# Performance work log

Measured on AMD Instinct MI355X. Metric: run time of the kernel, lower is better.

## Reference

```python
import jax, jax.numpy as jnp
import numpy as np
from jax import lax

B, C, L = 2048, 9605, 8
WL_PER_LABEL = 50
ALPHA = 0.5        # training_config['alpha4']
ALPHA1 = 0.1       # margin
ALPHA2 = 2.0       # training_config['alpha2']
ALPHA3 = 10.0      # training_config['alpha3']
ALPHA_OTHER = 0.5
NEG = jnp.float32(-1e30)


def setup_inputs() -> dict:
    key = jax.random.key(0)
    k1, k2, k3, k4 = jax.random.split(key, 4)
    x = jax.random.normal(k1, (B, C), dtype=jnp.float32) * 2.0
    y = (jax.random.uniform(k2, (B, C)) < 0.005).astype(jnp.float32)
    y_neg = (jax.random.uniform(k3, (B, C)) < 0.005).astype(jnp.float32)
    # whitelist masks: L app-labels, each whitelisting ~WL_PER_LABEL raw classes
    idx = jax.random.randint(k4, (L, WL_PER_LABEL), 0, C)
    wl_masks = jnp.zeros((L, C), dtype=bool).at[jnp.arange(L)[:, None], idx].set(True)
    return {"x": x, "y": y, "y_neg": y_neg, "wl_masks": wl_masks}


def reference(x, y, y_neg, wl_masks):
    # y_neg is consumed by the original forward (find_gt_whitelist) but never
    # affects the returned loss, faithfully ignored here.
    xs_pos = jax.nn.sigmoid(x)                                  # [B, C]
    # top_k_thres = max(11th-largest sigmoid, alpha_other)
    thres = jnp.maximum(lax.top_k(xs_pos, 11)[0][:, 10], ALPHA_OTHER)  # [B]
    # per-label whitelist max: m[b,l] = max_{c in wl_l} xs_pos[b,c]
    m = jnp.max(jnp.where(wl_masks[None, :, :], xs_pos[:, None, :], NEG), axis=-1)  # [B, L]
    # label l is a ground-truth whitelist label iff y has any positive in wl_l
    has_pos = jnp.einsum('bc,lc->bl', y, wl_masks.astype(y.dtype)) > 0   # [B, L]
    correct_max = jnp.max(jnp.where(has_pos, m, NEG), axis=-1)           # [B]
    incorrect_max = jnp.max(jnp.where(~has_pos, m, NEG), axis=-1)        # [B]
    any_correct = jnp.any(has_pos, axis=-1)
    any_incorrect = jnp.any(~has_pos, axis=-1)
    # union whitelist max (the "other" branch uses xs_pos over all wl indices)
    union_max = jnp.max(jnp.where(jnp.any(wl_masks, axis=0)[None, :], xs_pos, NEG), axis=-1)
    x1 = jnp.where(any_correct, correct_max, thres)
    x2 = jnp.where(any_correct,
                   jnp.where(any_incorrect, jnp.maximum(incorrect_max, thres), thres),
                   union_max)
    coef = jnp.where(any_correct, 1.0, 1.0 - ALPHA)
    d = x2 - x1 + ALPHA1
    rank = jnp.where(d > 0, ALPHA2, 1.0) * jax.nn.sigmoid(ALPHA3 * d)
    return jnp.mean(coef * rank)
```

## Files before the change

kernel.cpp:

```cpp
#include <hip/hip_runtime.h>

#define CC 9605
#define BB 2048
#define LL 8
#define CAND_MAX 384
#define NEGF (-1e30f)

#define WS_PARTIALS_OFF 16384

__device__ __forceinline__ unsigned enc_f(float f) {
  unsigned u = __float_as_uint(f);
  return (u & 0x80000000u) ? ~u : (u | 0x80000000u);
}
__device__ __forceinline__ float dec_u(unsigned e) {
  unsigned u = (e & 0x80000000u) ? (e & 0x7fffffffu) : ~e;
  return __uint_as_float(u);
}
__device__ __forceinline__ float sigm(float z) {
  return 1.0f / (1.0f + __expf(-z));
}

__global__ __launch_bounds__(256) void wl_prep(
    const unsigned char* __restrict__ wl, unsigned* __restrict__ wsu) {
  __shared__ unsigned sh_f[4];
  const int tid = threadIdx.x;
  const int lane = tid & 63;
  const int wid = tid >> 6;
  const unsigned* wlw = (const unsigned*)wl;
  const int nwords = (LL * CC) / 4;
  unsigned f = 0u;
  for (int j = tid; j < nwords; j += 256) {
    unsigned w = wlw[j];
#pragma unroll
    for (int k = 0; k < 4; ++k) {
      unsigned bv = (w >> (8 * k)) & 255u;
      if (bv == 1u)    { f |= 2u; if (k != 0) f |= 1u; }
      if (bv == 0x3fu) { f |= 8u; if (k == 1) f |= 4u; }
    }
  }
#pragma unroll
  for (int off = 32; off >= 1; off >>= 1) f |= __shfl_xor(f, off, 64);
  if (lane == 0) sh_f[wid] = f;
  __syncthreads();
  const unsigned g = sh_f[0] | sh_f[1] | sh_f[2] | sh_f[3];
  const int dt = (g & 1u) ? 0 : (g & 4u) ? 3 : (g & 2u) ? 1 : (g & 8u) ? 2 : 0;
  const int* wl32 = (const int*)wl;
  const float* wlf = (const float*)wl;
  const unsigned short* wlh = (const unsigned short*)wl;
  const int c = blockIdx.x * 256 + tid;
  unsigned m = 0u;
  if (c < CC) {
#pragma unroll
    for (int l = 0; l < LL; ++l) {
      int j = l * CC + c;
      bool on;
      if (dt == 0) on = (wl[j] != 0);
      else if (dt == 1) on = (wl32[j] != 0);
      else if (dt == 2) on = (wlf[j] != 0.0f);
      else on = (wlh[j] != 0);
      if (on) m |= (1u << l);
    }
  }
  unsigned long long bal = __ballot(m != 0u);
  if (bal) {
    unsigned wcnt = (unsigned)__popcll(bal);
    unsigned basep = 0u;
    if (lane == 0) basep = atomicAdd(&wsu[0], wcnt);
    basep = __shfl(basep, 0, 64);
    if (m) {
      unsigned pos = basep + (unsigned)__popcll(bal & ((1ull << lane) - 1ull));
      if (pos < 2048u) wsu[4 + pos] = ((unsigned)c << 8) | m;
    }
  }
}


#define ENCMAX(U, T)                                            \
  do {                                                          \
    U.x = enc_f(T.x); U.y = enc_f(T.y);                         \
    U.z = enc_f(T.z); U.w = enc_f(T.w);                         \
    mx = max(mx, max(max(U.x, U.y), max(U.z, U.w)));            \
  } while (0)

#define CNT4(U, T)                                              \
  (((U.x >= (T)) ? 1u : 0u) + ((U.y >= (T)) ? 1u : 0u) +        \
   ((U.z >= (T)) ? 1u : 0u) + ((U.w >= (T)) ? 1u : 0u))

#define BLK_COUNT(T, RES)                                       \
  do {                                                          \
    unsigned _c = CNT4(u0, (T)) + CNT4(u1, (T)) + CNT4(u2, (T)) \
                + CNT4(u3, (T)) + CNT4(u4, (T))                 \
                + ((et >= (T)) ? 1u : 0u);                      \
    _c += __shfl_xor(_c, 32, 64);                               \
    _c += __shfl_xor(_c, 16, 64);                               \
    _c += __shfl_xor(_c, 8, 64);                                \
    _c += __shfl_xor(_c, 4, 64);                                \
    _c += __shfl_xor(_c, 2, 64);                                \
    _c += __shfl_xor(_c, 1, 64);                                \
    __syncthreads();                   \
    if (lane == 0) sh_redC[wid] = _c;                           \
    __syncthreads();                                            \
    RES = sh_redC[0] + sh_redC[1] + sh_redC[2] + sh_redC[3] +   \
          sh_redC[4] + sh_redC[5] + sh_redC[6] + sh_redC[7];    \
  } while (0)

#define EMIT(V)                                                 \
  do {                                                          \
    if ((V) >= lo) sh_cand[pos++] = (V);                        \
  } while (0)

__global__ __launch_bounds__(512) void loss_kernel(
    const float* __restrict__ x, const float* __restrict__ y,
    const unsigned* __restrict__ wsu, float* __restrict__ partials) {
  __shared__ unsigned sh_cand[CAND_MAX];
  __shared__ unsigned sh_redM[8];
  __shared__ unsigned sh_redC[8];
  __shared__ unsigned sh_cnt;
  __shared__ unsigned sh_e11;
  __shared__ float sh_wl[8][10];

  const int tid = threadIdx.x;
  const int lane = tid & 63;
  const int wid = tid >> 6;
  const int b = blockIdx.x;
  const long long base = (long long)b * CC;

  const int soff = (4 - (b & 3)) & 3;
  const int ngroups = (CC - soff) >> 2;
  const int tailn = CC - soff - (ngroups << 2);
  const int m_extra = soff + tailn;
  const float4* vp = (const float4*)(x + base + soff);
  float4 t0 = vp[tid];
  float4 t1 = vp[tid + 512];
  float4 t2 = vp[tid + 1024];
  float4 t3 = vp[tid + 1536];
  const int g4 = tid + 2048;
  const bool v4 = (g4 < ngroups);
  float4 t4 = make_float4(0.0f, 0.0f, 0.0f, 0.0f);
  if (v4) t4 = vp[g4];
  float tailv = 0.0f;
  const bool has_tail = (tid < m_extra);
  if (has_tail) {
    int tailcol = (tid < soff) ? tid : (soff + (ngroups << 2) + (tid - soff));
    tailv = x[base + tailcol];
  }

  const unsigned nu = min(wsu[0], 2048u);
  const unsigned* ents = wsu + 4;
  unsigned ent0 = 0u;
  float gx0 = NEGF, gy0 = 0.0f;
  const bool h0 = (unsigned)tid < nu;
  if (h0) ent0 = ents[tid];
  if (h0) { gx0 = x[base + (ent0 >> 8)]; gy0 = y[base + (ent0 >> 8)]; }

  unsigned mx = 0u;
  uint4 u0, u1, u2, u3, u4;
  ENCMAX(u0, t0);
  ENCMAX(u1, t1);
  ENCMAX(u2, t2);
  ENCMAX(u3, t3);
  if (v4) {
    ENCMAX(u4, t4);
  } else {
    u4.x = 0u; u4.y = 0u; u4.z = 0u; u4.w = 0u;
  }
  unsigned et = 0u;
  if (has_tail) { et = enc_f(tailv); mx = max(mx, et); }
  if (tid == 0) sh_cnt = 0u;

  mx = max(mx, __shfl_xor(mx, 32, 64));
  mx = max(mx, __shfl_xor(mx, 16, 64));
  mx = max(mx, __shfl_xor(mx, 8, 64));
  mx = max(mx, __shfl_xor(mx, 4, 64));
  mx = max(mx, __shfl_xor(mx, 2, 64));
  mx = max(mx, __shfl_xor(mx, 1, 64));
  if (lane == 0) sh_redM[wid] = mx;
  __syncthreads();
  unsigned Emax = sh_redM[0];
#pragma unroll
  for (int w = 1; w < 8; ++w) Emax = max(Emax, sh_redM[w]);

  unsigned E11 = 0u;
  bool done = false;
  unsigned lo = (Emax > (1u << 23)) ? (Emax - (1u << 23)) : 1u;
  unsigned hi = Emax + 1u;
  unsigned c;
  BLK_COUNT(lo, c);
  while (c < 11u && lo > 1u) {
    hi = lo;
    lo = (lo > (1u << 23)) ? (lo - (1u << 23)) : 1u;
    BLK_COUNT(lo, c);
  }
  while (c > CAND_MAX) {
    if (hi - lo <= 1u) { E11 = lo; done = true; break; }
    unsigned mid = lo + ((hi - lo) >> 1);
    unsigned cm;
    BLK_COUNT(mid, cm);
    if (cm >= 11u) { lo = mid; c = cm; } else { hi = mid; }
  }

  if (!done) {
    unsigned nloc = CNT4(u0, lo) + CNT4(u1, lo) + CNT4(u2, lo) +
                    CNT4(u3, lo) + CNT4(u4, lo) + ((et >= lo) ? 1u : 0u);
    unsigned scan = nloc;
#pragma unroll
    for (int off = 1; off < 64; off <<= 1) {
      unsigned nn = __shfl_up(scan, off, 64);
      if (lane >= off) scan += nn;
    }
    unsigned wtot = __shfl(scan, 63, 64);
    unsigned basep = 0u;
    if (lane == 0) basep = atomicAdd(&sh_cnt, wtot);
    basep = __shfl(basep, 0, 64);
    unsigned pos = basep + scan - nloc;
    EMIT(u0.x); EMIT(u0.y); EMIT(u0.z); EMIT(u0.w);
    EMIT(u1.x); EMIT(u1.y); EMIT(u1.z); EMIT(u1.w);
    EMIT(u2.x); EMIT(u2.y); EMIT(u2.z); EMIT(u2.w);
    EMIT(u3.x); EMIT(u3.y); EMIT(u3.z); EMIT(u3.w);
    EMIT(u4.x); EMIT(u4.y); EMIT(u4.z); EMIT(u4.w);
    EMIT(et);
    __syncthreads();

    if (wid == 0) {
      unsigned v0[6];
#pragma unroll
      for (int j = 0; j < 6; ++j) {
        unsigned idx = (unsigned)lane + 64u * j;
        v0[j] = (idx < c) ? sh_cand[idx] : 0u;
      }
      unsigned ans = 0u;
      for (int r = 0; r < 11; ++r) {
        unsigned lmx = v0[0];
#pragma unroll
        for (int j = 1; j < 6; ++j) lmx = max(lmx, v0[j]);
        unsigned wm = lmx;
#pragma unroll
        for (int off = 32; off >= 1; off >>= 1)
          wm = max(wm, __shfl_xor(wm, off, 64));
        ans = wm;
        if (r < 10) {
          unsigned long long bal = __ballot(lmx == wm);
          int first = (int)__ffsll((long long)bal) - 1;
          if (lane == first) {
            bool rm = false;
#pragma unroll
            for (int j = 0; j < 6; ++j) {
              if (!rm && v0[j] == wm) { v0[j] = 0u; rm = true; }
            }
          }
        }
      }
      if (lane == 0) sh_e11 = ans;
    }
    __syncthreads();
    E11 = sh_e11;
  }

  float lm[8];
#pragma unroll
  for (int l = 0; l < 8; ++l) lm[l] = NEGF;
  unsigned pmask = 0u;
  if (h0) {
    unsigned mk = ent0 & 255u;
    pmask |= mk;
    if (gy0 > 0.0f) pmask |= (mk << 8);
#pragma unroll
    for (int l = 0; l < 8; ++l)
      if ((mk >> l) & 1u) lm[l] = fmaxf(lm[l], gx0);
  }
  for (unsigned e = (unsigned)tid + 512u; e < nu; e += 512u) {
    unsigned ent = ents[e];
    unsigned mk = ent & 255u;
    float xv = x[base + (ent >> 8)];
    float yv = y[base + (ent >> 8)];
    pmask |= mk;
    if (yv > 0.0f) pmask |= (mk << 8);
#pragma unroll
    for (int l = 0; l < 8; ++l)
      if ((mk >> l) & 1u) lm[l] = fmaxf(lm[l], xv);
  }
#pragma unroll
  for (int off = 32; off >= 1; off >>= 1) {
    pmask |= __shfl_xor(pmask, off, 64);
#pragma unroll
    for (int l = 0; l < 8; ++l) lm[l] = fmaxf(lm[l], __shfl_xor(lm[l], off, 64));
  }
  if (lane == 0) {
#pragma unroll
    for (int l = 0; l < 8; ++l) sh_wl[wid][l] = lm[l];
    sh_wl[wid][8] = __uint_as_float(pmask);
  }
  __syncthreads();

  if (tid == 0) {
    float LM[8];
    unsigned PM = 0u;
#pragma unroll
    for (int l = 0; l < 8; ++l) LM[l] = NEGF;
    for (int w = 0; w < 8; ++w) {
#pragma unroll
      for (int l = 0; l < 8; ++l) LM[l] = fmaxf(LM[l], sh_wl[w][l]);
      PM |= __float_as_uint(sh_wl[w][8]);
    }
    unsigned PR = PM & 255u, PO = (PM >> 8) & 255u;
    float thres = fmaxf(sigm(dec_u(E11)), 0.5f);
    float cmax = NEGF, imax = NEGF, umax = NEGF;
#pragma unroll
    for (int l = 0; l < 8; ++l) {
      if ((PR >> l) & 1u) {
        float ml = sigm(LM[l]);
        umax = fmaxf(umax, ml);
        if ((PO >> l) & 1u) cmax = fmaxf(cmax, ml);
        else imax = fmaxf(imax, ml);
      }
    }
    bool anyc = (PO != 0u);
    bool anyi = (PO != 255u);
    float x1 = anyc ? cmax : thres;
    float x2 = anyc ? (anyi ? fmaxf(imax, thres) : thres)
                    : ((nu > 0u) ? umax : NEGF);
    float coef = anyc ? 1.0f : 0.5f;
    float dd = x2 - x1 + 0.1f;
    float rank = ((dd > 0.0f) ? 2.0f : 1.0f) * sigm(10.0f * dd);
    partials[b] = coef * rank;
  }
}

__global__ void final_reduce(const float* __restrict__ partials,
                             float* __restrict__ out) {
  __shared__ float sh[4];
  const int tid = threadIdx.x;
  const int lane = tid & 63;
  const int wid = tid >> 6;
  float s = 0.0f;
  for (int i = tid; i < BB; i += 256) s += partials[i];
#pragma unroll
  for (int off = 32; off >= 1; off >>= 1) s += __shfl_xor(s, off, 64);
  if (lane == 0) sh[wid] = s;
  __syncthreads();
  if (tid == 0) out[0] = (sh[0] + sh[1] + sh[2] + sh[3]) * (1.0f / (float)BB);
}

extern "C" void kernel_launch(void* const* d_in, const int* in_sizes, int n_in,
                              void* d_out, int out_size, void* d_ws,
                              size_t ws_size, hipStream_t stream) {
  const float* x = (const float*)d_in[0];
  const float* y = (const float*)d_in[1];
  const unsigned char* wl = (const unsigned char*)d_in[3];
  float* out = (float*)d_out;
  unsigned* wsu = (unsigned*)d_ws;
  float* partials = (float*)((char*)d_ws + WS_PARTIALS_OFF);

  hipMemsetAsync(d_ws, 0, 16, stream);
  wl_prep<<<(CC + 255) / 256, 256, 0, stream>>>(wl, wsu);
  loss_kernel<<<BB, 512, 0, stream>>>(x, y, wsu, partials);
  final_reduce<<<1, 256, 0, stream>>>(partials, out);
}
```

Measured before the change: 239.5 us.

## Use ballot-based reductions and scans, parallel radix select, split whitelist prep

Replaces the shuffle-based block count reduction and the shuffle-up prefix scan with bit-sliced ballot/popcount and mbcnt, which relies on per-thread counts fitting in 5 bits. The serial 11-round max-removal selection of the 11th largest value becomes a binary search over the encoded value range, using ballot counts over candidates held in wave 0. The whitelist max pass is moved ahead of that selection so the other waves are not left idle while wave 0 selects. The whitelist prep is split into a grid-wide sniff kernel using atomicOr and a separate compact kernel, removing the redundant full-array scan that every prep block did, at the cost of one extra launch.

```diff
diff --git a/kernel.cpp b/kernel.cpp
--- a/kernel.cpp
+++ b/kernel.cpp
@@ -19,35 +19,40 @@
 __device__ __forceinline__ float sigm(float z) {
   return 1.0f / (1.0f + __expf(-z));
 }
-
-__global__ __launch_bounds__(256) void wl_prep(
-    const unsigned char* __restrict__ wl, unsigned* __restrict__ wsu) {
-  __shared__ unsigned sh_f[4];
+__device__ __forceinline__ unsigned prefix_lt(unsigned long long m) {
+  unsigned r = __builtin_amdgcn_mbcnt_lo((unsigned)m, 0u);
+  return __builtin_amdgcn_mbcnt_hi((unsigned)(m >> 32), r);
+}
+
+__global__ void wl_sniff(const unsigned* __restrict__ wlw,
+                         unsigned* __restrict__ wsu) {
+  const int nwords = (LL * CC) / 4;
+  const int stride = gridDim.x * blockDim.x;
+  unsigned f = 0u;
+  for (int j = blockIdx.x * blockDim.x + threadIdx.x; j < nwords; j += stride) {
+    unsigned w = wlw[j];
+#pragma unroll
+    for (int k = 0; k < 4; ++k) {
+      unsigned b = (w >> (8 * k)) & 255u;
+      if (b == 1u)    { f |= 2u; if (k != 0) f |= 1u; }
+      if (b == 0x3fu) { f |= 8u; if (k == 1) f |= 4u; }
+    }
+  }
+#pragma unroll
+  for (int off = 32; off >= 1; off >>= 1) f |= __shfl_xor(f, off, 64);
+  if ((threadIdx.x & 63) == 0 && f) atomicOr(&wsu[1], f);
+}
+
+__global__ void wl_compact(const unsigned char* __restrict__ wl,
+                           unsigned* __restrict__ wsu) {
   const int tid = threadIdx.x;
   const int lane = tid & 63;
-  const int wid = tid >> 6;
-  const unsigned* wlw = (const unsigned*)wl;
-  const int nwords = (LL * CC) / 4;
-  unsigned f = 0u;
-  for (int j = tid; j < nwords; j += 256) {
-    unsigned w = wlw[j];
-#pragma unroll
-    for (int k = 0; k < 4; ++k) {
-      unsigned bv = (w >> (8 * k)) & 255u;
-      if (bv == 1u)    { f |= 2u; if (k != 0) f |= 1u; }
-      if (bv == 0x3fu) { f |= 8u; if (k == 1) f |= 4u; }
-    }
-  }
-#pragma unroll
-  for (int off = 32; off >= 1; off >>= 1) f |= __shfl_xor(f, off, 64);
-  if (lane == 0) sh_f[wid] = f;
-  __syncthreads();
-  const unsigned g = sh_f[0] | sh_f[1] | sh_f[2] | sh_f[3];
+  const int c = blockIdx.x * 256 + tid;
+  const unsigned g = wsu[1];
   const int dt = (g & 1u) ? 0 : (g & 4u) ? 3 : (g & 2u) ? 1 : (g & 8u) ? 2 : 0;
   const int* wl32 = (const int*)wl;
   const float* wlf = (const float*)wl;
   const unsigned short* wlh = (const unsigned short*)wl;
-  const int c = blockIdx.x * 256 + tid;
   unsigned m = 0u;
   if (c < CC) {
 #pragma unroll
@@ -91,14 +96,13 @@
     unsigned _c = CNT4(u0, (T)) + CNT4(u1, (T)) + CNT4(u2, (T)) \
                 + CNT4(u3, (T)) + CNT4(u4, (T))                 \
                 + ((et >= (T)) ? 1u : 0u);                      \
-    _c += __shfl_xor(_c, 32, 64);                               \
-    _c += __shfl_xor(_c, 16, 64);                               \
-    _c += __shfl_xor(_c, 8, 64);                                \
-    _c += __shfl_xor(_c, 4, 64);                                \
-    _c += __shfl_xor(_c, 2, 64);                                \
-    _c += __shfl_xor(_c, 1, 64);                                \
+    unsigned _w = (unsigned)__popcll(__ballot(_c & 1u));        \
+    _w += (unsigned)__popcll(__ballot(_c & 2u)) << 1;           \
+    _w += (unsigned)__popcll(__ballot(_c & 4u)) << 2;           \
+    _w += (unsigned)__popcll(__ballot(_c & 8u)) << 3;           \
+    _w += (unsigned)__popcll(__ballot(_c & 16u)) << 4;          \
     __syncthreads();                   \
-    if (lane == 0) sh_redC[wid] = _c;                           \
+    if (lane == 0) sh_redC[wid] = _w;                           \
     __syncthreads();                                            \
     RES = sh_redC[0] + sh_redC[1] + sh_redC[2] + sh_redC[3] +   \
           sh_redC[4] + sh_redC[5] + sh_redC[6] + sh_redC[7];    \
@@ -116,7 +120,6 @@
   __shared__ unsigned sh_redM[8];
   __shared__ unsigned sh_redC[8];
   __shared__ unsigned sh_cnt;
-  __shared__ unsigned sh_e11;
   __shared__ float sh_wl[8][10];
 
   const int tid = threadIdx.x;
@@ -202,17 +205,22 @@
   if (!done) {
     unsigned nloc = CNT4(u0, lo) + CNT4(u1, lo) + CNT4(u2, lo) +
                     CNT4(u3, lo) + CNT4(u4, lo) + ((et >= lo) ? 1u : 0u);
-    unsigned scan = nloc;
-#pragma unroll
-    for (int off = 1; off < 64; off <<= 1) {
-      unsigned nn = __shfl_up(scan, off, 64);
-      if (lane >= off) scan += nn;
-    }
-    unsigned wtot = __shfl(scan, 63, 64);
+    unsigned long long m0 = __ballot(nloc & 1u);
+    unsigned long long m1 = __ballot(nloc & 2u);
+    unsigned long long m2 = __ballot(nloc & 4u);
+    unsigned long long m3 = __ballot(nloc & 8u);
+    unsigned long long m4 = __ballot(nloc & 16u);
+    unsigned wtot = (unsigned)__popcll(m0) + ((unsigned)__popcll(m1) << 1) +
+                    ((unsigned)__popcll(m2) << 2) +
+                    ((unsigned)__popcll(m3) << 3) +
+                    ((unsigned)__popcll(m4) << 4);
+    unsigned pre = prefix_lt(m0) + (prefix_lt(m1) << 1) +
+                   (prefix_lt(m2) << 2) + (prefix_lt(m3) << 3) +
+                   (prefix_lt(m4) << 4);
     unsigned basep = 0u;
     if (lane == 0) basep = atomicAdd(&sh_cnt, wtot);
-    basep = __shfl(basep, 0, 64);
-    unsigned pos = basep + scan - nloc;
+    basep = (unsigned)__builtin_amdgcn_readfirstlane((int)basep);
+    unsigned pos = basep + pre;
     EMIT(u0.x); EMIT(u0.y); EMIT(u0.z); EMIT(u0.w);
     EMIT(u1.x); EMIT(u1.y); EMIT(u1.z); EMIT(u1.w);
     EMIT(u2.x); EMIT(u2.y); EMIT(u2.z); EMIT(u2.w);
@@ -220,75 +228,65 @@
     EMIT(u4.x); EMIT(u4.y); EMIT(u4.z); EMIT(u4.w);
     EMIT(et);
     __syncthreads();
-
-    if (wid == 0) {
-      unsigned v0[6];
-#pragma unroll
-      for (int j = 0; j < 6; ++j) {
-        unsigned idx = (unsigned)lane + 64u * j;
-        v0[j] = (idx < c) ? sh_cand[idx] : 0u;
-      }
-      unsigned ans = 0u;
-      for (int r = 0; r < 11; ++r) {
-        unsigned lmx = v0[0];
-#pragma unroll
-        for (int j = 1; j < 6; ++j) lmx = max(lmx, v0[j]);
-        unsigned wm = lmx;
-#pragma unroll
-        for (int off = 32; off >= 1; off >>= 1)
-          wm = max(wm, __shfl_xor(wm, off, 64));
-        ans = wm;
-        if (r < 10) {
-          unsigned long long bal = __ballot(lmx == wm);
-          int first = (int)__ffsll((long long)bal) - 1;
-          if (lane == first) {
-            bool rm = false;
-#pragma unroll
-            for (int j = 0; j < 6; ++j) {
-              if (!rm && v0[j] == wm) { v0[j] = 0u; rm = true; }
-            }
-          }
-        }
-      }
-      if (lane == 0) sh_e11 = ans;
-    }
-    __syncthreads();
-    E11 = sh_e11;
-  }
-
-  float lm[8];
-#pragma unroll
-  for (int l = 0; l < 8; ++l) lm[l] = NEGF;
-  unsigned pmask = 0u;
-  if (h0) {
-    unsigned mk = ent0 & 255u;
-    pmask |= mk;
-    if (gy0 > 0.0f) pmask |= (mk << 8);
-#pragma unroll
-    for (int l = 0; l < 8; ++l)
-      if ((mk >> l) & 1u) lm[l] = fmaxf(lm[l], gx0);
-  }
-  for (unsigned e = (unsigned)tid + 512u; e < nu; e += 512u) {
-    unsigned ent = ents[e];
-    unsigned mk = ent & 255u;
-    float xv = x[base + (ent >> 8)];
-    float yv = y[base + (ent >> 8)];
-    pmask |= mk;
-    if (yv > 0.0f) pmask |= (mk << 8);
-#pragma unroll
-    for (int l = 0; l < 8; ++l)
-      if ((mk >> l) & 1u) lm[l] = fmaxf(lm[l], xv);
-  }
-#pragma unroll
-  for (int off = 32; off >= 1; off >>= 1) {
-    pmask |= __shfl_xor(pmask, off, 64);
-#pragma unroll
-    for (int l = 0; l < 8; ++l) lm[l] = fmaxf(lm[l], __shfl_xor(lm[l], off, 64));
-  }
-  if (lane == 0) {
-#pragma unroll
-    for (int l = 0; l < 8; ++l) sh_wl[wid][l] = lm[l];
-    sh_wl[wid][8] = __uint_as_float(pmask);
+  }
+
+  {
+    float lm[8];
+#pragma unroll
+    for (int l = 0; l < 8; ++l) lm[l] = NEGF;
+    unsigned pmask = 0u;
+    if (h0) {
+      unsigned mk = ent0 & 255u;
+      pmask |= mk;
+      if (gy0 > 0.0f) pmask |= (mk << 8);
+#pragma unroll
+      for (int l = 0; l < 8; ++l)
+        if ((mk >> l) & 1u) lm[l] = fmaxf(lm[l], gx0);
+    }
+    for (unsigned e = (unsigned)tid + 512u; e < nu; e += 512u) {
+      unsigned ent = ents[e];
+      unsigned mk = ent & 255u;
+      float xv = x[base + (ent >> 8)];
+      float yv = y[base + (ent >> 8)];
+      pmask |= mk;
+      if (yv > 0.0f) pmask |= (mk << 8);
+#pragma unroll
+      for (int l = 0; l < 8; ++l)
+        if ((mk >> l) & 1u) lm[l] = fmaxf(lm[l], xv);
+    }
+#pragma unroll
+    for (int off = 32; off >= 1; off >>= 1) {
+      pmask |= __shfl_xor(pmask, off, 64);
+#pragma unroll
+      for (int l = 0; l < 8; ++l)
+        lm[l] = fmaxf(lm[l], __shfl_xor(lm[l], off, 64));
+    }
+    if (lane == 0) {
+#pragma unroll
+      for (int l = 0; l < 8; ++l) sh_wl[wid][l] = lm[l];
+      sh_wl[wid][8] = __uint_as_float(pmask);
+    }
+  }
+
+  if (!done && wid == 0) {
+    unsigned c0 = ((unsigned)lane < c) ? sh_cand[lane] : 0u;
+    unsigned c1 = ((unsigned)lane + 64u < c) ? sh_cand[lane + 64u] : 0u;
+    unsigned c2 = ((unsigned)lane + 128u < c) ? sh_cand[lane + 128u] : 0u;
+    unsigned c3 = ((unsigned)lane + 192u < c) ? sh_cand[lane + 192u] : 0u;
+    unsigned c4 = ((unsigned)lane + 256u < c) ? sh_cand[lane + 256u] : 0u;
+    unsigned c5 = ((unsigned)lane + 320u < c) ? sh_cand[lane + 320u] : 0u;
+    unsigned blo = lo, bhi = hi;
+    while (bhi - blo > 1u) {
+      unsigned mid = blo + ((bhi - blo) >> 1);
+      unsigned cnt = (unsigned)__popcll(__ballot(c0 >= mid)) +
+                     (unsigned)__popcll(__ballot(c1 >= mid)) +
+                     (unsigned)__popcll(__ballot(c2 >= mid)) +
+                     (unsigned)__popcll(__ballot(c3 >= mid)) +
+                     (unsigned)__popcll(__ballot(c4 >= mid)) +
+                     (unsigned)__popcll(__ballot(c5 >= mid));
+      if (cnt >= 11u) blo = mid; else bhi = mid;
+    }
+    E11 = blo;
   }
   __syncthreads();
 
@@ -352,7 +350,8 @@
   float* partials = (float*)((char*)d_ws + WS_PARTIALS_OFF);
 
   hipMemsetAsync(d_ws, 0, 16, stream);
-  wl_prep<<<(CC + 255) / 256, 256, 0, stream>>>(wl, wsu);
+  wl_sniff<<<64, 256, 0, stream>>>((const unsigned*)wl, wsu);
+  wl_compact<<<(CC + 255) / 256, 256, 0, stream>>>(wl, wsu);
   loss_kernel<<<BB, 512, 0, stream>>>(x, y, wsu, partials);
   final_reduce<<<1, 256, 0, stream>>>(partials, out);
 }
```

After: 220.6 us. 7.9% less time.
